# Optimization experiments

Measured on AMD Instinct MI355X. Metric: run time of the kernel, lower is better.

The kernel has to match this reference:

```python
import jax, jax.numpy as jnp
import numpy as np

N = 50000        # nodes
E_RAND = 800000  # random edges (self-loops appended -> E = 850000)
H = 8            # num_heads
D = 32           # h_feat_dim
IN = 128         # in_feat_dim
SM = 256         # sm_dim
SP = 128         # sp_dim
NEG_SLOPE = 0.2  # DGL GATv2Conv default


def setup_inputs() -> dict:
    key = jax.random.key(0)
    ks = jax.random.split(key, 16)
    s = 0.05
    self_loops = jnp.arange(N, dtype=jnp.int32)
    return {
        "sm_feats": jax.random.normal(ks[0], (N, SM), jnp.float32),
        "sp_feats": jax.random.normal(ks[1], (N, SP), jnp.float32),
        "src": jnp.concatenate([jax.random.randint(ks[2], (E_RAND,), 0, N, jnp.int32), self_loops]),
        "dst": jnp.concatenate([jax.random.randint(ks[3], (E_RAND,), 0, N, jnp.int32), self_loops]),
        # T1 / T2 linears
        "T1_w": jax.random.normal(ks[4], (SM, IN), jnp.float32) * s,
        "T1_b": jnp.zeros((IN,), jnp.float32),
        "T2_w": jax.random.normal(ks[5], (SP, IN), jnp.float32) * s,
        "T2_b": jnp.zeros((IN,), jnp.float32),
        # GATv2 layer 1: in = 2*IN
        "g1_src_w": jax.random.normal(ks[6], (2 * IN, H * D), jnp.float32) * s,
        "g1_dst_w": jax.random.normal(ks[7], (2 * IN, H * D), jnp.float32) * s,
        "g1_attn": jax.random.normal(ks[8], (H, D), jnp.float32) * s,
        "g1_bias": jnp.zeros((H * D,), jnp.float32),
        # GATv2 layer 2: in = D (after head-mean)
        "g2_src_w": jax.random.normal(ks[9], (D, H * D), jnp.float32) * s,
        "g2_dst_w": jax.random.normal(ks[10], (D, H * D), jnp.float32) * s,
        "g2_attn": jax.random.normal(ks[11], (H, D), jnp.float32) * s,
        "g2_bias": jnp.zeros((H * D,), jnp.float32),
    }


def gatv2_conv(x, src, dst, w_src, w_dst, attn, bias):
    # DGL GATv2Conv (share_weights=False, bias=True, no residual/activation)
    feat_src = (x @ w_src).reshape(-1, H, D)   # [N,H,D]
    feat_dst = (x @ w_dst).reshape(-1, H, D)   # [N,H,D]
    e = jax.nn.leaky_relu(feat_src[src] + feat_dst[dst], NEG_SLOPE)  # [E,H,D]
    score = jnp.einsum('ehd,hd->eh', e, attn)  # [E,H]
    # edge softmax over incoming edges per destination (self-loops ensure non-empty)
    smax = jax.ops.segment_max(score, dst, num_segments=N)           # [N,H]
    ex = jnp.exp(score - smax[dst])
    denom = jax.ops.segment_sum(ex, dst, num_segments=N)             # [N,H]
    alpha = ex / denom[dst]                                          # [E,H]
    out = jax.ops.segment_sum(alpha[:, :, None] * feat_src[src], dst, num_segments=N)  # [N,H,D]
    return out + bias.reshape(1, H, D)


def reference(sm_feats, sp_feats, src, dst,
              T1_w, T1_b, T2_w, T2_b,
              g1_src_w, g1_dst_w, g1_attn, g1_bias,
              g2_src_w, g2_dst_w, g2_attn, g2_bias):
    in_feat = jnp.concatenate([sm_feats @ T1_w + T1_b,
                               sp_feats @ T2_w + T2_b], axis=1)      # [N, 2*IN]
    h = gatv2_conv(in_feat, src, dst, g1_src_w, g1_dst_w, g1_attn, g1_bias)
    h = jax.nn.elu(h).mean(axis=1)                                   # [N, D]
    h = gatv2_conv(h, src, dst, g2_src_w, g2_dst_w, g2_attn, g2_bias)
    return h.mean(axis=1)                                            # [N, D]
```

## Files before the change

kernel.cpp:

```cpp
#include <hip/hip_runtime.h>
#include <hip/hip_fp16.h>


typedef unsigned int uint32;
typedef unsigned short u16;
typedef float f32x4 __attribute__((ext_vector_type(4)));
typedef _Float16 f16x2 __attribute__((ext_vector_type(2)));
typedef _Float16 f16x4 __attribute__((ext_vector_type(4)));
typedef _Float16 f16x8 __attribute__((ext_vector_type(8)));

union H2 { f16x2 v; uint32 u; };

__device__ __forceinline__ int wave_incl_scan(int x) {
  int lane = threadIdx.x & 63;
#pragma unroll
  for (int off = 1; off < 64; off <<= 1) {
    int t = __shfl_up(x, off, 64);
    if (lane >= off) x += t;
  }
  return x;
}

__global__ __launch_bounds__(256) void k_deg(const int* __restrict__ dst, int* __restrict__ deg, int E) {
  int e = blockIdx.x * 256 + threadIdx.x;
  if (e < E) atomicAdd(&deg[dst[e]], 1);
}

__global__ __launch_bounds__(1024) void k_scan1(const int* __restrict__ deg, int* __restrict__ rp,
                                                int n, int Etot) {
  __shared__ int wpart[16];
  __shared__ int sbase;
  int tid = threadIdx.x, lane = tid & 63, wid = tid >> 6;
  if (tid == 0) sbase = 0;
  __syncthreads();
  for (int c0 = 0; c0 < n; c0 += 4096) {
    int i0 = c0 + tid * 4;
    int v0 = 0, v1 = 0, v2 = 0, v3 = 0;
    if (i0 + 3 < n) {
      int4 t = *(const int4*)(deg + i0);
      v0 = t.x; v1 = t.y; v2 = t.z; v3 = t.w;
    } else {
      if (i0 < n) v0 = deg[i0];
      if (i0 + 1 < n) v1 = deg[i0 + 1];
      if (i0 + 2 < n) v2 = deg[i0 + 2];
      if (i0 + 3 < n) v3 = deg[i0 + 3];
    }
    int ts = v0 + v1 + v2 + v3;
    int incl = wave_incl_scan(ts);
    if (lane == 63) wpart[wid] = incl;
    __syncthreads();
    if (wid == 0 && lane < 16) {
      int xv = wpart[lane];
#pragma unroll
      for (int off = 1; off < 16; off <<= 1) {
        int t = __shfl_up(xv, off, 64);
        if (lane >= off) xv += t;
      }
      wpart[lane] = xv;
    }
    __syncthreads();
    int tot = wpart[15];
    int base = sbase + (wid ? wpart[wid - 1] : 0);
    int excl = base + incl - ts;
    if (i0 + 3 < n) {
      int4 o; o.x = excl; o.y = excl + v0; o.z = excl + v0 + v1; o.w = excl + v0 + v1 + v2;
      *(int4*)(rp + i0) = o;
    } else {
      if (i0 < n) rp[i0] = excl;
      if (i0 + 1 < n) rp[i0 + 1] = excl + v0;
      if (i0 + 2 < n) rp[i0 + 2] = excl + v0 + v1;
      if (i0 + 3 < n) rp[i0 + 3] = excl + v0 + v1 + v2;
    }
    __syncthreads();
    if (tid == 0) sbase += tot;
  }
  if (tid == 0) rp[n] = Etot;
}

__global__ __launch_bounds__(256) void k_fill(const int* __restrict__ src, const int* __restrict__ dst,
                                              const int* __restrict__ rp, int* __restrict__ cnt,
                                              int* __restrict__ csr_src, int E) {
  int e = blockIdx.x * 256 + threadIdx.x;
  if (e < E) {
    int d = dst[e];
    int p = rp[d] + atomicAdd(&cnt[d], 1);
    csr_src[p] = src[e];
  }
}

__global__ __launch_bounds__(256) void k_precomb(const float* __restrict__ T1w, const float* __restrict__ T1b,
                                                 const float* __restrict__ T2w, const float* __restrict__ T2b,
                                                 const float* __restrict__ G1, const float* __restrict__ G2,
                                                 __half* __restrict__ Bf, float* __restrict__ cvec) {
  int bb = blockIdx.x;
  const float* G = (bb < 385) ? G1 : G2;
  int off = (bb < 385) ? 0 : 256;
  int r = (bb < 385) ? bb : bb - 385;
  int j = threadIdx.x;
  float acc = 0.f;
  if (r < 256) {
    for (int m = 0; m < 128; m++) acc += T1w[r * 128 + m] * G[m * 256 + j];
  } else if (r < 384) {
    int rr = r - 256;
    for (int m = 0; m < 128; m++) acc += T2w[rr * 128 + m] * G[(128 + m) * 256 + j];
  } else {
    for (int m = 0; m < 128; m++) acc += T1b[m] * G[m * 256 + j] + T2b[m] * G[(128 + m) * 256 + j];
    cvec[off + j] = acc;
    return;
  }
  int k = r, colabs = off + j;
  int kt = k >> 5, lq = (k >> 3) & 3, j8 = k & 7;
  int cb = colabs >> 7, colr = colabs & 127, ni = colr >> 4, lr = colr & 15;
  size_t idx = ((size_t)(((cb * 12 + kt) * 8 + ni) * 4 + lq) * 16 + lr) * 8 + j8;
  Bf[idx] = __float2half(acc);
}

#define GLL(GP, LP)                                                     \
  __builtin_amdgcn_global_load_lds(                                     \
      (const __attribute__((address_space(1))) void*)(GP),              \
      (__attribute__((address_space(3))) void*)(LP), 16, 0, 0)

__global__ __launch_bounds__(256, 4) void k_gemm(const float* __restrict__ sm, const float* __restrict__ sp,
                                                 const u16* __restrict__ Bf, const float* __restrict__ cvec,
                                                 __half* __restrict__ fs, __half* __restrict__ fd, int N) {
  __shared__ u16 BFl[3 * 4096];
  __shared__ u16 AFl[2 * 4096];
  int tid = threadIdx.x, w = tid >> 6, l = tid & 63;
  int lr = l & 15, lq = l >> 4;
  int L = blockIdx.x;
  int x = L & 7, m = L >> 3;
  int cb = m & 3;
  int rb = x + 8 * (m >> 2);
  int col0 = cb * 128, row0 = rb * 128;
  if (row0 >= N) return;

  int o_sm[4], o_sp[4], woff[4];
#pragma unroll
  for (int i = 0; i < 4; i++) {
    int idx = i * 256 + tid;
    int r = idx >> 3, c8 = idx & 7;
    int rg = row0 + r; if (rg >= N) rg = N - 1;
    o_sm[i] = rg * 256 + c8 * 4;
    o_sp[i] = rg * 128 + c8 * 4;
    woff[i] = r * 32 + ((c8 * 4) ^ ((r & 6) << 2));
  }
  int r0l = w * 32 + lr, r1l = r0l + 16;
  int ra0 = r0l * 32 + ((lq * 8) ^ ((r0l & 6) << 2));
  int ra1 = r1l * 32 + ((lq * 8) ^ ((r1l & 6) << 2));

  f32x4 acc[2][8];
#pragma unroll
  for (int mt = 0; mt < 2; mt++)
#pragma unroll
    for (int ni = 0; ni < 8; ni++) acc[mt][ni] = (f32x4){0.f, 0.f, 0.f, 0.f};

#define STAGE_B(S, BUF)                                                 \
  {                                                                     \
    size_t g0 = (size_t)(cb * 12 + (S)) * 4096;                         \
    _Pragma("unroll") for (int i = 0; i < 2; i++) {                     \
      int c = i * 256 + tid;                                            \
      int lb = (BUF)*4096 + (i * 4 + w) * 512;                          \
      GLL(Bf + g0 + (size_t)c * 8, &BFl[lb]);                           \
    }                                                                   \
  }

#define ALOAD(S)                                                        \
  {                                                                     \
    _Pragma("unroll") for (int i = 0; i < 4; i++) {                     \
      const float* g = ((S) < 8) ? (sm + o_sm[i] + (S)*32) : (sp + o_sp[i] + ((S)-8) * 32); \
      D[i] = *(const float4*)g;                                         \
    }                                                                   \
  }

#define AWRITE(SLOT)                                                    \
  {                                                                     \
    _Pragma("unroll") for (int i = 0; i < 4; i++) {                     \
      f16x4 h;                                                          \
      h[0] = (_Float16)D[i].x; h[1] = (_Float16)D[i].y;                 \
      h[2] = (_Float16)D[i].z; h[3] = (_Float16)D[i].w;                 \
      *(f16x4*)&AFl[(SLOT)*4096 + woff[i]] = h;                         \
    }                                                                   \
  }

  float4 D[4];
  ALOAD(0);
  STAGE_B(0, 0);
  STAGE_B(1, 1);
  asm volatile("s_waitcnt vmcnt(4)" ::: "memory");
  AWRITE(0);
  asm volatile("s_waitcnt vmcnt(2)" ::: "memory");
  asm volatile("s_waitcnt lgkmcnt(0)" ::: "memory");
  __builtin_amdgcn_sched_barrier(0);
  __builtin_amdgcn_s_barrier();

#pragma unroll
  for (int st = 0; st < 12; st++) {
    const int cu = st & 1, nx = cu ^ 1, bs = st % 3;
    if (st < 11) ALOAD(st + 1);
    if (st < 10) STAGE_B(st + 2, (st + 2) % 3);
    f16x8 a0 = *(const f16x8*)&AFl[cu * 4096 + ra0];
    f16x8 a1 = *(const f16x8*)&AFl[cu * 4096 + ra1];
#pragma unroll
    for (int ni = 0; ni < 8; ni++) {
      f16x8 bf = *(const f16x8*)&BFl[bs * 4096 + (ni * 64 + l) * 8];
      acc[0][ni] = __builtin_amdgcn_mfma_f32_16x16x32_f16(a0, bf, acc[0][ni], 0, 0, 0);
      acc[1][ni] = __builtin_amdgcn_mfma_f32_16x16x32_f16(a1, bf, acc[1][ni], 0, 0, 0);
    }
    if (st < 10) {
      asm volatile("s_waitcnt vmcnt(2)" ::: "memory");
    } else if (st == 10) {
      asm volatile("s_waitcnt vmcnt(0)" ::: "memory");
    }
    if (st < 11) {
      AWRITE(nx);
      asm volatile("s_waitcnt lgkmcnt(0)" ::: "memory");
      __builtin_amdgcn_sched_barrier(0);
      __builtin_amdgcn_s_barrier();
    }
  }

#pragma unroll
  for (int mt = 0; mt < 2; mt++) {
    int rbr = row0 + w * 32 + mt * 16 + lq * 4;
#pragma unroll
    for (int ni = 0; ni < 8; ni++) {
      int c = col0 + ni * 16 + lr;
      float cv = cvec[c];
      __half* op = fs; int cc = c;
      if (c >= 256) { op = fd; cc = c - 256; }
#pragma unroll
      for (int r = 0; r < 4; r++) {
        int rr = rbr + r;
        if (rr < N) op[(size_t)rr * 256 + cc] = __float2half(acc[mt][ni][r] + cv);
      }
    }
  }
#undef STAGE_B
#undef ALOAD
#undef AWRITE
}

__global__ __launch_bounds__(256) void k_feat2(const float* __restrict__ h, const float* __restrict__ Ws,
                                               const float* __restrict__ Wd, __half* __restrict__ fs,
                                               __half* __restrict__ fd, int N) {
  int j = threadIdx.x;
  int n0 = blockIdx.x * 32;
  float ws[32], wd[32];
#pragma unroll
  for (int k = 0; k < 32; k++) {
    ws[k] = Ws[k * 256 + j];
    wd[k] = Wd[k * 256 + j];
  }
  int nend = n0 + 32; if (nend > N) nend = N;
#pragma unroll 2
  for (int n = n0; n < nend; n++) {
    const float* hr = h + (size_t)n * 32;
    float as = 0.f, ad = 0.f;
#pragma unroll
    for (int k = 0; k < 32; k++) {
      float hv = hr[k];
      as += hv * ws[k];
      ad += hv * wd[k];
    }
    fs[(size_t)n * 256 + j] = __float2half(as);
    fd[(size_t)n * 256 + j] = __float2half(ad);
  }
}

template <int FINAL>
__global__ __launch_bounds__(256) void k_edge(const uint4* __restrict__ fs4, const uint4* __restrict__ fd4,
                                              const int* __restrict__ csr_src, const int* __restrict__ rp,
                                              const float* __restrict__ attn, const float* __restrict__ bias,
                                              float* __restrict__ out, int N) {
  int n = blockIdx.x * 4 + (threadIdx.x >> 6);
  if (n >= N) return;
  int lane = threadIdx.x & 63;
  int lh = lane & 31;
  float4 a0 = ((const float4*)attn)[lh * 2];
  float4 a1 = ((const float4*)attn)[lh * 2 + 1];
  H2 AV01, AV23, AV45, AV67;
  AV01.v = (f16x2){(_Float16)a0.x, (_Float16)a0.y};
  AV23.v = (f16x2){(_Float16)a0.z, (_Float16)a0.w};
  AV45.v = (f16x2){(_Float16)a1.x, (_Float16)a1.y};
  AV67.v = (f16x2){(_Float16)a1.z, (_Float16)a1.w};
  const f16x2 c02 = {(_Float16)0.2f, (_Float16)0.2f};
  uint4 yu = fd4[(size_t)n * 32 + lh];
  H2 Y01, Y23, Y45, Y67;
  Y01.u = yu.x; Y23.u = yu.y; Y45.u = yu.z; Y67.u = yu.w;
  int beg = rp[n], end = rp[n + 1];
  float den = 0.f;
  float acc[8] = {0.f, 0.f, 0.f, 0.f, 0.f, 0.f, 0.f, 0.f};

  auto pair1 = [&](uint4 xu, bool tail) {
    H2 Xa, Xb, Xc, Xd;
    Xa.u = xu.x; Xb.u = xu.y; Xc.u = xu.z; Xd.u = xu.w;
    f16x2 e0 = Xa.v + Y01.v, e1 = Xb.v + Y23.v, e2 = Xc.v + Y45.v, e3 = Xd.v + Y67.v;
    f16x2 t0 = __builtin_elementwise_max(e0, e0 * c02);
    f16x2 t1 = __builtin_elementwise_max(e1, e1 * c02);
    f16x2 t2 = __builtin_elementwise_max(e2, e2 * c02);
    f16x2 t3 = __builtin_elementwise_max(e3, e3 * c02);
    float p = __builtin_amdgcn_fdot2(t0, AV01.v, 0.f, false);
    p = __builtin_amdgcn_fdot2(t1, AV23.v, p, false);
    p = __builtin_amdgcn_fdot2(t2, AV45.v, p, false);
    p = __builtin_amdgcn_fdot2(t3, AV67.v, p, false);
    p += __shfl_xor(p, 1, 64);
    p += __shfl_xor(p, 2, 64);
    float wgt = __expf(p);
    if (tail && lane >= 32) wgt = 0.f;
    den += wgt;
    acc[0] += wgt * (float)Xa.v.x; acc[1] += wgt * (float)Xa.v.y;
    acc[2] += wgt * (float)Xb.v.x; acc[3] += wgt * (float)Xb.v.y;
    acc[4] += wgt * (float)Xc.v.x; acc[5] += wgt * (float)Xc.v.y;
    acc[6] += wgt * (float)Xd.v.x; acc[7] += wgt * (float)Xd.v.y;
  };

  int e = beg;
  int np = (end - beg) >> 1;
  if (np > 0) {
    int sA = csr_src[e], sB = csr_src[e + 1];
    int s = (lane < 32) ? sA : sB;
    uint4 xcur = fs4[(size_t)s * 32 + lh];
    for (int q = 1; q < np; q++) {
      int eb = e + 2 * q;
      int tA = csr_src[eb], tB = csr_src[eb + 1];
      int t = (lane < 32) ? tA : tB;
      uint4 xnext = fs4[(size_t)t * 32 + lh];
      pair1(xcur, false);
      xcur = xnext;
    }
    pair1(xcur, false);
    e += 2 * np;
  }
  if (e < end) {
    int sA = csr_src[e];
    uint4 xu = fs4[(size_t)sA * 32 + lh];
    pair1(xu, true);
  }

  den += __shfl_xor(den, 32, 64);
#pragma unroll
  for (int j = 0; j < 8; j++) acc[j] += __shfl_xor(acc[j], 32, 64);
  float invd = 1.f / den;
  float4 b0 = ((const float4*)bias)[lh * 2];
  float4 b1 = ((const float4*)bias)[lh * 2 + 1];
  float bj[8] = {b0.x, b0.y, b0.z, b0.w, b1.x, b1.y, b1.z, b1.w};
#pragma unroll
  for (int j = 0; j < 8; j++) {
    float v = acc[j] * invd + bj[j];
    if (!FINAL) v = v > 0.f ? v : expm1f(v);
    acc[j] = v;
  }
#pragma unroll
  for (int mask = 4; mask <= 16; mask <<= 1)
#pragma unroll
    for (int j = 0; j < 8; j++) acc[j] += __shfl_xor(acc[j], mask, 64);
  if (lane < 4) {
    float4 o0 = {acc[0] * 0.125f, acc[1] * 0.125f, acc[2] * 0.125f, acc[3] * 0.125f};
    float4 o1 = {acc[4] * 0.125f, acc[5] * 0.125f, acc[6] * 0.125f, acc[7] * 0.125f};
    ((float4*)out)[(size_t)n * 8 + lane * 2] = o0;
    ((float4*)out)[(size_t)n * 8 + lane * 2 + 1] = o1;
  }
}

extern "C" void kernel_launch(void* const* d_in, const int* in_sizes, int n_in,
                              void* d_out, int out_size, void* d_ws, size_t ws_size,
                              hipStream_t stream) {
  const float* sm  = (const float*)d_in[0];
  const float* sp  = (const float*)d_in[1];
  const int*   src = (const int*)d_in[2];
  const int*   dst = (const int*)d_in[3];
  const float* T1w = (const float*)d_in[4];
  const float* T1b = (const float*)d_in[5];
  const float* T2w = (const float*)d_in[6];
  const float* T2b = (const float*)d_in[7];
  const float* g1sw = (const float*)d_in[8];
  const float* g1dw = (const float*)d_in[9];
  const float* g1a  = (const float*)d_in[10];
  const float* g1b  = (const float*)d_in[11];
  const float* g2sw = (const float*)d_in[12];
  const float* g2dw = (const float*)d_in[13];
  const float* g2a  = (const float*)d_in[14];
  const float* g2b  = (const float*)d_in[15];
  const int N = in_sizes[1] / 128;
  const int E = in_sizes[2];
  float* out = (float*)d_out;

  size_t off = 0;
  char* wsb = (char*)d_ws;
  auto alloc = [&](size_t bytes) -> void* {
    void* p = wsb + off;
    off += (bytes + 255) & ~(size_t)255;
    return p;
  };
  __half* Bf  = (__half*)alloc((size_t)512 * 384 * 2);
  float* cvec  = (float*)alloc(512 * 4);
  int* deg     = (int*)alloc((size_t)N * 4);
  int* cnt     = (int*)alloc((size_t)N * 4);
  int* row_ptr = (int*)alloc((size_t)(N + 1) * 4);
  int* csr_src = (int*)alloc((size_t)E * 4);
  __half* fs   = (__half*)alloc((size_t)N * 256 * 2);
  __half* fd   = (__half*)alloc((size_t)N * 256 * 2);
  float* hmid  = (float*)alloc((size_t)N * 32 * 4);
  (void)ws_size; (void)n_in; (void)out_size;

  (void)hipMemsetAsync(deg, 0, (size_t)N * 4, stream);
  (void)hipMemsetAsync(cnt, 0, (size_t)N * 4, stream);

  k_deg<<<(E + 255) / 256, 256, 0, stream>>>(dst, deg, E);
  k_scan1<<<1, 1024, 0, stream>>>(deg, row_ptr, N, E);
  k_fill<<<(E + 255) / 256, 256, 0, stream>>>(src, dst, row_ptr, cnt, csr_src, E);

  k_precomb<<<770, 256, 0, stream>>>(T1w, T1b, T2w, T2b, g1sw, g1dw, Bf, cvec);

  int rbs = (N + 127) / 128;
  int rbp = (rbs + 7) & ~7;
  k_gemm<<<dim3(rbp * 4), 256, 0, stream>>>(sm, sp, (const u16*)Bf, cvec, fs, fd, N);
  k_edge<0><<<(N + 3) / 4, 256, 0, stream>>>((const uint4*)fs, (const uint4*)fd, csr_src, row_ptr, g1a, g1b, hmid, N);

  k_feat2<<<(N + 31) / 32, 256, 0, stream>>>(hmid, g2sw, g2dw, fs, fd, N);
  k_edge<1><<<(N + 3) / 4, 256, 0, stream>>>((const uint4*)fs, (const uint4*)fd, csr_src, row_ptr, g2a, g2b, out, N);
}
```

Baseline: 460.9 us.

## Store layer-1 features head-sliced and run a per-head edge kernel

The GEMM epilogue now writes source and destination features in a head-major layout ([H][N][32]). A new layer-1 edge kernel processes one head per block, eight nodes at a time, with each quarter-wave handling one edge so a gather fetches only 64 bytes for that head. Per-head ELU results are written in place into the destination buffer, and a separate kernel averages the eight heads into hmid. The aim is better gather locality and per-lane efficiency on the dominant edge pass, at the cost of an extra combine kernel and of interleaving all heads across concurrently running blocks.

```diff
diff --git a/kernel.cpp b/kernel.cpp
--- a/kernel.cpp
+++ b/kernel.cpp
@@ -120,6 +120,7 @@
       (const __attribute__((address_space(1))) void*)(GP),              \
       (__attribute__((address_space(3))) void*)(LP), 16, 0, 0)
 
+template <int HSLICED>
 __global__ __launch_bounds__(256, 4) void k_gemm(const float* __restrict__ sm, const float* __restrict__ sp,
                                                  const u16* __restrict__ Bf, const float* __restrict__ cvec,
                                                  __half* __restrict__ fs, __half* __restrict__ fd, int N) {
@@ -231,7 +232,11 @@
 #pragma unroll
       for (int r = 0; r < 4; r++) {
         int rr = rbr + r;
-        if (rr < N) op[(size_t)rr * 256 + cc] = __float2half(acc[mt][ni][r] + cv);
+        if (rr < N) {
+          size_t o = HSLICED ? (((size_t)(cc >> 5) * N + rr) * 32 + (cc & 31))
+                             : ((size_t)rr * 256 + cc);
+          op[o] = __float2half(acc[mt][ni][r] + cv);
+        }
       }
     }
   }
@@ -267,11 +272,110 @@
   }
 }
 
-template <int FINAL>
-__global__ __launch_bounds__(256) void k_edge(const uint4* __restrict__ fs4, const uint4* __restrict__ fd4,
-                                              const int* __restrict__ csr_src, const int* __restrict__ rp,
-                                              const float* __restrict__ attn, const float* __restrict__ bias,
-                                              float* __restrict__ out, int N) {
+__global__ __launch_bounds__(256) void k_edge1h(const u16* __restrict__ fsh, u16* fdh,
+                                                const int* __restrict__ csr_src, const int* __restrict__ rp,
+                                                const float* __restrict__ attn, const float* __restrict__ bias,
+                                                int N) {
+  int B = blockIdx.x;
+  int h = B & 7, g = B >> 3;
+  int lane = threadIdx.x & 63, wid = threadIdx.x >> 6;
+  int half = lane >> 5, hl = lane & 31, es = hl >> 2, q = hl & 3;
+  int nr = g * 8 + wid * 2 + half;
+  bool wvalid = nr < N;
+  int n = wvalid ? nr : N - 1;
+  int fo = q * 8;
+  size_t sbase = (size_t)h * N * 32;
+  size_t nbase = sbase + (size_t)n * 32 + fo;
+  uint4 yu = *(const uint4*)&fdh[nbase];
+  H2 Y0, Y1, Y2, Y3;
+  Y0.u = yu.x; Y1.u = yu.y; Y2.u = yu.z; Y3.u = yu.w;
+  const float* ap = attn + h * 32 + fo;
+  float4 a0 = *(const float4*)ap;
+  float4 a1 = *(const float4*)(ap + 4);
+  H2 A0, A1, A2, A3;
+  A0.v = (f16x2){(_Float16)a0.x, (_Float16)a0.y};
+  A1.v = (f16x2){(_Float16)a0.z, (_Float16)a0.w};
+  A2.v = (f16x2){(_Float16)a1.x, (_Float16)a1.y};
+  A3.v = (f16x2){(_Float16)a1.z, (_Float16)a1.w};
+  const f16x2 c02 = {(_Float16)0.2f, (_Float16)0.2f};
+  int beg = rp[n], end = rp[n + 1];
+  float den = 0.f;
+  float acc[8] = {0.f, 0.f, 0.f, 0.f, 0.f, 0.f, 0.f, 0.f};
+
+  for (int eb = beg; eb < end; eb += 8) {
+    int ei = eb + es;
+    int sv = (ei < end) ? ei : beg;
+    int s = csr_src[sv];
+    uint4 xu = *(const uint4*)&fsh[sbase + (size_t)s * 32 + fo];
+    H2 X0, X1, X2, X3;
+    X0.u = xu.x; X1.u = xu.y; X2.u = xu.z; X3.u = xu.w;
+    f16x2 e0 = X0.v + Y0.v, e1 = X1.v + Y1.v, e2 = X2.v + Y2.v, e3 = X3.v + Y3.v;
+    f16x2 t0 = __builtin_elementwise_max(e0, e0 * c02);
+    f16x2 t1 = __builtin_elementwise_max(e1, e1 * c02);
+    f16x2 t2 = __builtin_elementwise_max(e2, e2 * c02);
+    f16x2 t3 = __builtin_elementwise_max(e3, e3 * c02);
+    float p = __builtin_amdgcn_fdot2(t0, A0.v, 0.f, false);
+    p = __builtin_amdgcn_fdot2(t1, A1.v, p, false);
+    p = __builtin_amdgcn_fdot2(t2, A2.v, p, false);
+    p = __builtin_amdgcn_fdot2(t3, A3.v, p, false);
+    p += __shfl_xor(p, 1, 64);
+    p += __shfl_xor(p, 2, 64);
+    float wgt = __expf(p);
+    if (ei >= end) wgt = 0.f;
+    den += wgt;
+    acc[0] += wgt * (float)X0.v.x; acc[1] += wgt * (float)X0.v.y;
+    acc[2] += wgt * (float)X1.v.x; acc[3] += wgt * (float)X1.v.y;
+    acc[4] += wgt * (float)X2.v.x; acc[5] += wgt * (float)X2.v.y;
+    acc[6] += wgt * (float)X3.v.x; acc[7] += wgt * (float)X3.v.y;
+  }
+#pragma unroll
+  for (int mk = 4; mk <= 16; mk <<= 1) {
+    den += __shfl_xor(den, mk, 64);
+#pragma unroll
+    for (int j = 0; j < 8; j++) acc[j] += __shfl_xor(acc[j], mk, 64);
+  }
+  float invd = 1.f / den;
+  const float* bp = bias + h * 32 + fo;
+  float4 b0 = *(const float4*)bp;
+  float4 b1 = *(const float4*)(bp + 4);
+  float bj[8] = {b0.x, b0.y, b0.z, b0.w, b1.x, b1.y, b1.z, b1.w};
+  float v[8];
+#pragma unroll
+  for (int j = 0; j < 8; j++) {
+    float t = acc[j] * invd + bj[j];
+    v[j] = t > 0.f ? t : expm1f(t);
+  }
+  if (es == 0 && wvalid) {
+    H2 P0, P1, P2, P3;
+    P0.v = (f16x2){(_Float16)v[0], (_Float16)v[1]};
+    P1.v = (f16x2){(_Float16)v[2], (_Float16)v[3]};
+    P2.v = (f16x2){(_Float16)v[4], (_Float16)v[5]};
+    P3.v = (f16x2){(_Float16)v[6], (_Float16)v[7]};
+    uint4 st = {P0.u, P1.u, P2.u, P3.u};
+    *(uint4*)&fdh[nbase] = st;
+  }
+}
+
+__global__ __launch_bounds__(256) void k_comb16(const u16* __restrict__ p, float* __restrict__ o, int N) {
+  int idx = blockIdx.x * 256 + threadIdx.x;
+  if (idx >= N * 8) return;
+  size_t base = (size_t)idx * 4;
+  size_t stride = (size_t)N * 32;
+  float s0 = 0.f, s1 = 0.f, s2 = 0.f, s3 = 0.f;
+#pragma unroll
+  for (int h = 0; h < 8; h++) {
+    uint2 u = *(const uint2*)&p[h * stride + base];
+    H2 a, b; a.u = u.x; b.u = u.y;
+    s0 += (float)a.v.x; s1 += (float)a.v.y; s2 += (float)b.v.x; s3 += (float)b.v.y;
+  }
+  float4 r = {s0 * 0.125f, s1 * 0.125f, s2 * 0.125f, s3 * 0.125f};
+  *(float4*)&o[base] = r;
+}
+
+__global__ __launch_bounds__(256) void k_edge2(const uint4* __restrict__ fs4, const uint4* __restrict__ fd4,
+                                               const int* __restrict__ csr_src, const int* __restrict__ rp,
+                                               const float* __restrict__ attn, const float* __restrict__ bias,
+                                               float* __restrict__ out, int N) {
   int n = blockIdx.x * 4 + (threadIdx.x >> 6);
   if (n >= N) return;
   int lane = threadIdx.x & 63;
@@ -345,11 +449,7 @@
   float4 b1 = ((const float4*)bias)[lh * 2 + 1];
   float bj[8] = {b0.x, b0.y, b0.z, b0.w, b1.x, b1.y, b1.z, b1.w};
 #pragma unroll
-  for (int j = 0; j < 8; j++) {
-    float v = acc[j] * invd + bj[j];
-    if (!FINAL) v = v > 0.f ? v : expm1f(v);
-    acc[j] = v;
-  }
+  for (int j = 0; j < 8; j++) acc[j] = acc[j] * invd + bj[j];
 #pragma unroll
   for (int mask = 4; mask <= 16; mask <<= 1)
 #pragma unroll
@@ -414,9 +514,11 @@
 
   int rbs = (N + 127) / 128;
   int rbp = (rbs + 7) & ~7;
-  k_gemm<<<dim3(rbp * 4), 256, 0, stream>>>(sm, sp, (const u16*)Bf, cvec, fs, fd, N);
-  k_edge<0><<<(N + 3) / 4, 256, 0, stream>>>((const uint4*)fs, (const uint4*)fd, csr_src, row_ptr, g1a, g1b, hmid, N);
+  k_gemm<1><<<dim3(rbp * 4), 256, 0, stream>>>(sm, sp, (const u16*)Bf, cvec, fs, fd, N);
+  int egrid = ((N + 7) / 8) * 8;
+  k_edge1h<<<egrid, 256, 0, stream>>>((const u16*)fs, (u16*)fd, csr_src, row_ptr, g1a, g1b, N);
+  k_comb16<<<(N * 8 + 255) / 256, 256, 0, stream>>>((const u16*)fd, hmid, N);
 
   k_feat2<<<(N + 31) / 32, 256, 0, stream>>>(hmid, g2sw, g2dw, fs, fd, N);
-  k_edge<1><<<(N + 3) / 4, 256, 0, stream>>>((const uint4*)fs, (const uint4*)fd, csr_src, row_ptr, g2a, g2b, out, N);
-}
+  k_edge2<<<(N + 3) / 4, 256, 0, stream>>>((const uint4*)fs, (const uint4*)fd, csr_src, row_ptr, g2a, g2b, out, N);
+}
```

Result: slower. 536.7 us (+16.5%).

## Merge CSR build kernels into precombine and GEMM launches to overlap work

Applied to the files above, without the earlier changes.

Folds the degree-count atomics into the weight-precombine kernel as extra blocks, and the CSR fill into the GEMM kernel as trailing blocks, which removes two launches and lets the independent graph-building work overlap with compute. It also vectorizes the h row loads in k_feat2 as float4. The gemm kernel's LDS and launch bounds now also apply to the fill blocks, which may limit their occupancy and add contention with GEMM blocks.

```diff
diff --git a/kernel.cpp b/kernel.cpp
--- a/kernel.cpp
+++ b/kernel.cpp
@@ -19,11 +19,6 @@
     if (lane >= off) x += t;
   }
   return x;
-}
-
-__global__ __launch_bounds__(256) void k_deg(const int* __restrict__ dst, int* __restrict__ deg, int E) {
-  int e = blockIdx.x * 256 + threadIdx.x;
-  if (e < E) atomicAdd(&deg[dst[e]], 1);
 }
 
 __global__ __launch_bounds__(1024) void k_scan1(const int* __restrict__ deg, int* __restrict__ rp,
@@ -77,26 +72,21 @@
   if (tid == 0) rp[n] = Etot;
 }
 
-__global__ __launch_bounds__(256) void k_fill(const int* __restrict__ src, const int* __restrict__ dst,
-                                              const int* __restrict__ rp, int* __restrict__ cnt,
-                                              int* __restrict__ csr_src, int E) {
-  int e = blockIdx.x * 256 + threadIdx.x;
-  if (e < E) {
-    int d = dst[e];
-    int p = rp[d] + atomicAdd(&cnt[d], 1);
-    csr_src[p] = src[e];
-  }
-}
-
-__global__ __launch_bounds__(256) void k_precomb(const float* __restrict__ T1w, const float* __restrict__ T1b,
-                                                 const float* __restrict__ T2w, const float* __restrict__ T2b,
-                                                 const float* __restrict__ G1, const float* __restrict__ G2,
-                                                 __half* __restrict__ Bf, float* __restrict__ cvec) {
+__global__ __launch_bounds__(256) void k_predeg(const float* __restrict__ T1w, const float* __restrict__ T1b,
+                                                const float* __restrict__ T2w, const float* __restrict__ T2b,
+                                                const float* __restrict__ G1, const float* __restrict__ G2,
+                                                __half* __restrict__ Bf, float* __restrict__ cvec,
+                                                const int* __restrict__ dst, int* __restrict__ deg, int E) {
   int bb = blockIdx.x;
+  int j = threadIdx.x;
+  if (bb >= 770) {
+    int e = (bb - 770) * 256 + j;
+    if (e < E) atomicAdd(&deg[dst[e]], 1);
+    return;
+  }
   const float* G = (bb < 385) ? G1 : G2;
   int off = (bb < 385) ? 0 : 256;
   int r = (bb < 385) ? bb : bb - 385;
-  int j = threadIdx.x;
   float acc = 0.f;
   if (r < 256) {
     for (int m = 0; m < 128; m++) acc += T1w[r * 128 + m] * G[m * 256 + j];
@@ -120,12 +110,25 @@
       (const __attribute__((address_space(1))) void*)(GP),              \
       (__attribute__((address_space(3))) void*)(LP), 16, 0, 0)
 
-__global__ __launch_bounds__(256, 4) void k_gemm(const float* __restrict__ sm, const float* __restrict__ sp,
-                                                 const u16* __restrict__ Bf, const float* __restrict__ cvec,
-                                                 __half* __restrict__ fs, __half* __restrict__ fd, int N) {
+__global__ __launch_bounds__(256, 4) void k_gemmfill(const float* __restrict__ sm, const float* __restrict__ sp,
+                                                     const u16* __restrict__ Bf, const float* __restrict__ cvec,
+                                                     __half* __restrict__ fs, __half* __restrict__ fd, int N,
+                                                     int GB, const int* __restrict__ src,
+                                                     const int* __restrict__ dst, const int* __restrict__ rp,
+                                                     int* __restrict__ cnt, int* __restrict__ csr_src, int E) {
   __shared__ u16 BFl[3 * 4096];
   __shared__ u16 AFl[2 * 4096];
-  int tid = threadIdx.x, w = tid >> 6, l = tid & 63;
+  int tid = threadIdx.x;
+  if (blockIdx.x >= GB) {
+    int e = (blockIdx.x - GB) * 256 + tid;
+    if (e < E) {
+      int d = dst[e];
+      int p = rp[d] + atomicAdd(&cnt[d], 1);
+      csr_src[p] = src[e];
+    }
+    return;
+  }
+  int w = tid >> 6, l = tid & 63;
   int lr = l & 15, lq = l >> 4;
   int L = blockIdx.x;
   int x = L & 7, m = L >> 3;
@@ -254,13 +257,13 @@
   int nend = n0 + 32; if (nend > N) nend = N;
 #pragma unroll 2
   for (int n = n0; n < nend; n++) {
-    const float* hr = h + (size_t)n * 32;
+    const float4* hr4 = (const float4*)(h + (size_t)n * 32);
     float as = 0.f, ad = 0.f;
 #pragma unroll
-    for (int k = 0; k < 32; k++) {
-      float hv = hr[k];
-      as += hv * ws[k];
-      ad += hv * wd[k];
+    for (int kk = 0; kk < 8; kk++) {
+      float4 t = hr4[kk];
+      as += t.x * ws[4 * kk] + t.y * ws[4 * kk + 1] + t.z * ws[4 * kk + 2] + t.w * ws[4 * kk + 3];
+      ad += t.x * wd[4 * kk] + t.y * wd[4 * kk + 1] + t.z * wd[4 * kk + 2] + t.w * wd[4 * kk + 3];
     }
     fs[(size_t)n * 256 + j] = __float2half(as);
     fd[(size_t)n * 256 + j] = __float2half(ad);
@@ -406,15 +409,16 @@
   (void)hipMemsetAsync(deg, 0, (size_t)N * 4, stream);
   (void)hipMemsetAsync(cnt, 0, (size_t)N * 4, stream);
 
-  k_deg<<<(E + 255) / 256, 256, 0, stream>>>(dst, deg, E);
+  int DB = (E + 255) / 256;
+
+  k_predeg<<<770 + DB, 256, 0, stream>>>(T1w, T1b, T2w, T2b, g1sw, g1dw, Bf, cvec, dst, deg, E);
   k_scan1<<<1, 1024, 0, stream>>>(deg, row_ptr, N, E);
-  k_fill<<<(E + 255) / 256, 256, 0, stream>>>(src, dst, row_ptr, cnt, csr_src, E);
-
-  k_precomb<<<770, 256, 0, stream>>>(T1w, T1b, T2w, T2b, g1sw, g1dw, Bf, cvec);
 
   int rbs = (N + 127) / 128;
   int rbp = (rbs + 7) & ~7;
-  k_gemm<<<dim3(rbp * 4), 256, 0, stream>>>(sm, sp, (const u16*)Bf, cvec, fs, fd, N);
+  int GB = rbp * 4;
+  k_gemmfill<<<GB + DB, 256, 0, stream>>>(sm, sp, (const u16*)Bf, cvec, fs, fd, N,
+                                          GB, src, dst, row_ptr, cnt, csr_src, E);
   k_edge<0><<<(N + 3) / 4, 256, 0, stream>>>((const uint4*)fs, (const uint4*)fd, csr_src, row_ptr, g1a, g1b, hmid, N);
 
   k_feat2<<<(N + 31) / 32, 256, 0, stream>>>(hmid, g2sw, g2dw, fs, fd, N);
```

After: 428.9 us (median of 2 runs). -6.9%, faster.
